# Optimization experiments

Measured on AMD Instinct MI355X. Metric: run time of the kernel, lower is better.

The kernel has to match this reference:

```python
import jax, jax.numpy as jnp
import numpy as np

B, N, D, DN, F, NUM_F, O, H = 8, 4096, 256, 128, 128, 1024, 8, 1024
EPS = 1e-5

def setup_inputs() -> dict:
    key = jax.random.key(0)
    ks = jax.random.split(key, 10)
    s = 0.02
    x = jax.random.normal(ks[0], (B, N, D), dtype=jnp.float32)
    ctx = jax.random.normal(ks[1], (B, DN), dtype=jnp.float32)
    idx = jax.random.randint(ks[2], (F,), 0, NUM_F, dtype=jnp.int64)
    cond_w = jax.random.normal(ks[3], (DN, 2 * D), dtype=jnp.float32) * s
    cond_b = jnp.zeros((2 * D,), dtype=jnp.float32)
    ffn_w_in = jax.random.normal(ks[4], (D, 2 * H), dtype=jnp.float32) * s
    ffn_b_in = jnp.zeros((2 * H,), dtype=jnp.float32)
    ffn_w_out = jax.random.normal(ks[5], (H, D), dtype=jnp.float32) * s
    ffn_b_out = jnp.zeros((D,), dtype=jnp.float32)
    emb = jax.random.normal(ks[6], (NUM_F, D * O), dtype=jnp.float32) * s
    return {"x": x, "ctx": ctx, "idx": idx, "cond_w": cond_w, "cond_b": cond_b,
            "ffn_w_in": ffn_w_in, "ffn_b_in": ffn_b_in,
            "ffn_w_out": ffn_w_out, "ffn_b_out": ffn_b_out, "emb": emb}

def reference(x, ctx, idx, cond_w, cond_b, ffn_w_in, ffn_b_in, ffn_w_out, ffn_b_out, emb):
    # Conditional LayerNorm: normalize over last dim, FiLM-style modulation from ctx
    mu = jnp.mean(x, axis=-1, keepdims=True)
    var = jnp.mean((x - mu) ** 2, axis=-1, keepdims=True)
    h = (x - mu) * jax.lax.rsqrt(var + EPS)                      # [B,N,D]
    ss = ctx @ cond_w + cond_b                                   # [B,2D]
    scale, shift = jnp.split(ss, 2, axis=-1)                     # [B,D] each
    h = h * (1.0 + scale[:, None, :]) + shift[:, None, :]
    # Gated FFN: in-proj -> (gelu(gate) * value) -> out-proj
    uv = h @ ffn_w_in + ffn_b_in                                 # [B,N,2H]
    u, v = jnp.split(uv, 2, axis=-1)
    y = (jax.nn.gelu(u) * v) @ ffn_w_out + ffn_b_out             # [B,N,D]
    # Embedding-generated per-feature output weights, then batched contraction
    w = emb[idx].reshape(F, D, O)                                # gather [F,D,O]
    out = jnp.einsum('bnd,fdo->bnfo', y, w)                      # [B,N,F,O]
    return out
```

## Files before the change

kernel.cpp:

```cpp
#include <hip/hip_runtime.h>
#include <cstdint>
#include <cstddef>

#define M_TOT 32768
#define D_    256
#define DN_   128
#define TWO_D 512
#define H_    1024
#define TWO_H 2048

typedef unsigned short ushort_t;
typedef __attribute__((ext_vector_type(8))) short bf16x8;
typedef __attribute__((ext_vector_type(4))) float f32x4;

__device__ __forceinline__ ushort_t f2bf(float f) {
  union { float f; uint32_t i; } v; v.f = f;
  uint32_t r = v.i + 0x7fffu + ((v.i >> 16) & 1u);
  return (ushort_t)(r >> 16);
}

__device__ __forceinline__ void async_ld16(const void* g, void* l) {
  __builtin_amdgcn_global_load_lds(
      (const __attribute__((address_space(1))) void*)g,
      (__attribute__((address_space(3))) void*)l, 16, 0, 0);
}

__global__ __launch_bounds__(256) void cond_ss_kernel(
    const float* __restrict__ ctx, const float* __restrict__ cond_w,
    const float* __restrict__ cond_b, float* __restrict__ ss) {
  int j = blockIdx.x * 256 + threadIdx.x;
  int b = j >> 9, col = j & 511;
  float acc = cond_b[col];
  for (int k = 0; k < DN_; ++k)
    acc += ctx[b * DN_ + k] * cond_w[k * TWO_D + col];
  ss[j] = acc;
}

__global__ __launch_bounds__(256) void transpose_f32_bf16_kernel(
    const float* __restrict__ in, ushort_t* __restrict__ out, int R, int C) {
  __shared__ float T[64 * 65];
  int ctiles = C >> 6;
  int bi = blockIdx.x / ctiles, bj = blockIdx.x % ctiles;
  int r0 = bi * 64, c0 = bj * 64;
  int tid = threadIdx.x;
#pragma unroll
  for (int it = 0; it < 16; ++it) {
    int idx = it * 256 + tid;
    int r = idx >> 6, c = idx & 63;
    T[r * 65 + c] = in[(size_t)(r0 + r) * C + c0 + c];
  }
  __syncthreads();
#pragma unroll
  for (int it = 0; it < 8; ++it) {
    int idx = it * 256 + tid;
    int a = idx >> 5;
    int b = (idx & 31) * 2;
    uint32_t pk = (uint32_t)f2bf(T[b * 65 + a]) |
                  ((uint32_t)f2bf(T[(b + 1) * 65 + a]) << 16);
    *(uint32_t*)&out[(size_t)(c0 + a) * R + r0 + b] = pk;
  }
}

__global__ __launch_bounds__(256) void gather_emb_kernel(
    const float* __restrict__ emb, const int* __restrict__ idx,
    ushort_t* __restrict__ W2T) {
  int f = blockIdx.x;
  bool looks64 = (idx[1] == 0) & (idx[3] == 0) & (idx[5] == 0) & (idx[7] == 0);
  int fi = looks64 ? idx[2 * f] : idx[f];
  const float* src = emb + (size_t)fi * 2048;
  int o = threadIdx.x >> 5, d0 = (threadIdx.x & 31) * 8;
  ushort_t buf[8];
#pragma unroll
  for (int k = 0; k < 8; ++k) buf[k] = f2bf(src[(d0 + k) * 8 + o]);
  *(bf16x8*)&W2T[(size_t)(f * 8 + o) * 256 + d0] = *(bf16x8*)buf;
}

__global__ __launch_bounds__(256) void ln_film_kernel(
    const float* __restrict__ x, const float* __restrict__ ss,
    ushort_t* __restrict__ h) {
  int row = blockIdx.x * 4 + (threadIdx.x >> 6);
  int lane = threadIdx.x & 63;
  int b = row >> 12;
  const float* xr = x + (size_t)row * D_;
  float4 pk = *(const float4*)(xr + lane * 4);
  float f0 = pk.x, f1 = pk.y, f2 = pk.z, f3 = pk.w;
  float s = f0 + f1 + f2 + f3;
  float q = f0 * f0 + f1 * f1 + f2 * f2 + f3 * f3;
#pragma unroll
  for (int off = 32; off > 0; off >>= 1) {
    s += __shfl_xor(s, off, 64);
    q += __shfl_xor(q, off, 64);
  }
  float mean = s * (1.0f / 256.0f);
  float var = q * (1.0f / 256.0f) - mean * mean;
  float rs = rsqrtf(var + 1e-5f);
  int d = lane * 4;
  const float* ssb = ss + b * TWO_D;
  float o0 = (f0 - mean) * rs * (1.0f + ssb[d + 0]) + ssb[256 + d + 0];
  float o1 = (f1 - mean) * rs * (1.0f + ssb[d + 1]) + ssb[256 + d + 1];
  float o2 = (f2 - mean) * rs * (1.0f + ssb[d + 2]) + ssb[256 + d + 2];
  float o3 = (f3 - mean) * rs * (1.0f + ssb[d + 3]) + ssb[256 + d + 3];
  uint2 st;
  st.x = (uint32_t)f2bf(o0) | ((uint32_t)f2bf(o1) << 16);
  st.y = (uint32_t)f2bf(o2) | ((uint32_t)f2bf(o3) << 16);
  *(uint2*)(h + (size_t)row * D_ + lane * 4) = st;
}

__global__ __launch_bounds__(256, 2) void ffn_fused_kernel(
    const ushort_t* __restrict__ h,
    const ushort_t* __restrict__ WinT,
    const float* __restrict__ bin,
    const ushort_t* __restrict__ WoutT,
    const float* __restrict__ bout,
    ushort_t* __restrict__ y) {
  __shared__ ushort_t Sh[2][16384];
  __shared__ ushort_t Gs[64 * 72];
  const int tid = threadIdx.x, lane = tid & 63, wave = tid >> 6;
  const int r = lane >> 2, q = lane & 3;
  const int l15 = lane & 15, l4 = lane >> 4;
  const int m0 = blockIdx.x * 64;
  const int fragoff = l15 * 32 + l4 * 8;

  const char* winp  = (const char*)WinT  + (wave * 16 + r) * 512 + q * 16;
  const char* woutp = (const char*)WoutT + (size_t)wave * 32768 + r * 2048 + q * 16;

  const ushort_t* hp = h + (size_t)(m0 + wave * 16 + l15) * 256 + l4 * 8;
  bf16x8 a_reg[8];
#pragma unroll
  for (int kc = 0; kc < 8; ++kc) a_reg[kc] = *(const bf16x8*)(hp + kc * 32);

#pragma unroll
  for (int i = 0; i < 4; ++i) {
    int t = i * 4 + wave;
    async_ld16(winp + i * 64,          &Sh[0][t * 512]);
    async_ld16(winp + i * 64 + 524288, &Sh[0][(16 + t) * 512]);
  }

  f32x4 yac[16] = {};
  int pb = 0;

  for (int j = 0; j < 16; ++j) {
    const int jb = j * 32768;
    f32x4 uac[4] = {}, vac[4] = {};

    asm volatile("s_waitcnt vmcnt(0)" ::: "memory");
    __builtin_amdgcn_s_barrier();
    asm volatile("" ::: "memory");
    {
      ushort_t* nxt = Sh[pb ^ 1];
#pragma unroll
      for (int i = 0; i < 4; ++i) {
        int t = i * 4 + wave;
        async_ld16(winp + jb + 256 + i * 64,          &nxt[t * 512]);
        async_ld16(winp + jb + 256 + i * 64 + 524288, &nxt[(16 + t) * 512]);
      }
      const ushort_t* cur = Sh[pb];
      __builtin_amdgcn_s_setprio(1);
#pragma unroll
      for (int ks = 0; ks < 4; ++ks) {
        bf16x8 af = a_reg[ks];
#pragma unroll
        for (int jt = 0; jt < 4; ++jt) {
          bf16x8 bu = *(const bf16x8*)&cur[(ks * 4 + jt) * 512 + fragoff];
          bf16x8 bv = *(const bf16x8*)&cur[(16 + ks * 4 + jt) * 512 + fragoff];
          uac[jt] = __builtin_amdgcn_mfma_f32_16x16x32_bf16(af, bu, uac[jt], 0, 0, 0);
          vac[jt] = __builtin_amdgcn_mfma_f32_16x16x32_bf16(af, bv, vac[jt], 0, 0, 0);
        }
      }
      __builtin_amdgcn_s_setprio(0);
    }
    pb ^= 1;

    asm volatile("s_waitcnt vmcnt(0)" ::: "memory");
    __builtin_amdgcn_s_barrier();
    asm volatile("" ::: "memory");
    {
      ushort_t* nxt = Sh[pb ^ 1];
#pragma unroll
      for (int i = 0; i < 4; ++i) {
        int t = i * 4 + wave;
        async_ld16(woutp + (size_t)i * 131072 + j * 128,      &nxt[t * 512]);
        async_ld16(woutp + (size_t)i * 131072 + j * 128 + 64, &nxt[(16 + t) * 512]);
      }
      const ushort_t* cur = Sh[pb];
      __builtin_amdgcn_s_setprio(1);
#pragma unroll
      for (int ks = 0; ks < 4; ++ks) {
        bf16x8 af = a_reg[4 + ks];
#pragma unroll
        for (int jt = 0; jt < 4; ++jt) {
          bf16x8 bu = *(const bf16x8*)&cur[(ks * 4 + jt) * 512 + fragoff];
          bf16x8 bv = *(const bf16x8*)&cur[(16 + ks * 4 + jt) * 512 + fragoff];
          uac[jt] = __builtin_amdgcn_mfma_f32_16x16x32_bf16(af, bu, uac[jt], 0, 0, 0);
          vac[jt] = __builtin_amdgcn_mfma_f32_16x16x32_bf16(af, bv, vac[jt], 0, 0, 0);
        }
      }
      __builtin_amdgcn_s_setprio(0);
    }
    pb ^= 1;

    asm volatile("s_waitcnt vmcnt(0)" ::: "memory");
    __builtin_amdgcn_s_barrier();
    asm volatile("" ::: "memory");
    if (j < 15) {
      ushort_t* nxt = Sh[pb ^ 1];
#pragma unroll
      for (int i = 0; i < 4; ++i) {
        int t = i * 4 + wave;
        async_ld16(winp + jb + 32768 + i * 64,          &nxt[t * 512]);
        async_ld16(winp + jb + 32768 + i * 64 + 524288, &nxt[(16 + t) * 512]);
      }
    }
#pragma unroll
    for (int jt = 0; jt < 4; ++jt) {
      int col = jt * 16 + l15;
      float bub = bin[j * 64 + col];
      float bvb = bin[1024 + j * 64 + col];
#pragma unroll
      for (int rr = 0; rr < 4; ++rr) {
        float u = uac[jt][rr] + bub;
        float v = vac[jt][rr] + bvb;
        float t = 0.7978845608028654f * (u + 0.044715f * u * u * u);
        float e = __expf(2.0f * t);
        float th = 1.0f - 2.0f / (e + 1.0f);
        float gl = 0.5f * u * (1.0f + th);
        Gs[(wave * 16 + l4 * 4 + rr) * 72 + col] = f2bf(gl * v);
      }
    }
    {
      const ushort_t* cur = Sh[pb];
#pragma unroll
      for (int s2 = 0; s2 < 2; ++s2) {
        bf16x8 gf = *(const bf16x8*)&Gs[(wave * 16 + l15) * 72 + s2 * 32 + l4 * 8];
        __builtin_amdgcn_s_setprio(1);
#pragma unroll
        for (int nt = 0; nt < 16; ++nt) {
          bf16x8 bw = *(const bf16x8*)&cur[(s2 * 16 + nt) * 512 + fragoff];
          yac[nt] = __builtin_amdgcn_mfma_f32_16x16x32_bf16(gf, bw, yac[nt], 0, 0, 0);
        }
        __builtin_amdgcn_s_setprio(0);
      }
    }
    pb ^= 1;
  }

  asm volatile("s_waitcnt vmcnt(0)" ::: "memory");
  __builtin_amdgcn_s_barrier();
  asm volatile("" ::: "memory");
  ushort_t* E = &Sh[0][0];
#pragma unroll
  for (int nt = 0; nt < 16; ++nt) {
    int col = nt * 16 + l15;
    float bb = bout[col];
#pragma unroll
    for (int rr = 0; rr < 4; ++rr)
      E[(wave * 16 + l4 * 4 + rr) * 264 + col] = f2bf(yac[nt][rr] + bb);
  }
  asm volatile("s_waitcnt lgkmcnt(0)" ::: "memory");
  __builtin_amdgcn_s_barrier();
  asm volatile("" ::: "memory");
#pragma unroll
  for (int it = 0; it < 8; ++it) {
    int id = it * 256 + tid;
    int rr = id >> 5, cc = id & 31;
    bf16x8 vv = *(const bf16x8*)&E[rr * 264 + cc * 8];
    *(bf16x8*)&y[(size_t)(m0 + rr) * 256 + cc * 8] = vv;
  }
}

__global__ __launch_bounds__(256, 2) void gemm_out_kernel(
    const ushort_t* __restrict__ A, const ushort_t* __restrict__ BT,
    float* __restrict__ C) {
  __shared__ ushort_t As[128 * 64];
  __shared__ ushort_t Bs[128 * 64];
  __shared__ float Cs[64 * 132];
  const int tid = threadIdx.x, lane = tid & 63, wave = tid >> 6;
  const int wm = wave >> 1, wn = wave & 1;
  const int m0 = blockIdx.x * 128, n0 = blockIdx.y * 128;
  const int r = lane >> 2, q = lane & 3;
  const int l15 = lane & 15, l4 = lane >> 4;
  const int fragoff = l15 * 32 + l4 * 8;
  const int N = 1024, K = 256;
  f32x4 acc[4][4] = {};
  for (int k0 = 0; k0 < K; k0 += 64) {
    for (int t = wave; t < 16; t += 4) {
      int rt = t >> 1, ks = t & 1;
      async_ld16(A + (size_t)(m0 + rt * 16 + r) * K + k0 + ks * 32 + q * 8, &As[t * 512]);
      async_ld16(BT + (size_t)(n0 + rt * 16 + r) * K + k0 + ks * 32 + q * 8, &Bs[t * 512]);
    }
    __syncthreads();
#pragma unroll
    for (int ks = 0; ks < 2; ++ks) {
      bf16x8 a[4], b[4];
#pragma unroll
      for (int i = 0; i < 4; ++i)
        a[i] = *(const bf16x8*)&As[((wm * 4 + i) * 2 + ks) * 512 + fragoff];
#pragma unroll
      for (int jt = 0; jt < 4; ++jt)
        b[jt] = *(const bf16x8*)&Bs[((wn * 4 + jt) * 2 + ks) * 512 + fragoff];
#pragma unroll
      for (int i = 0; i < 4; ++i)
#pragma unroll
        for (int jt = 0; jt < 4; ++jt)
          acc[i][jt] = __builtin_amdgcn_mfma_f32_16x16x32_bf16(a[i], b[jt], acc[i][jt], 0, 0, 0);
    }
    __syncthreads();
  }
#pragma unroll
  for (int p = 0; p < 2; ++p) {
    __syncthreads();
    if (wm == p) {
#pragma unroll
      for (int jt = 0; jt < 4; ++jt) {
        int col = wn * 64 + jt * 16 + l15;
#pragma unroll
        for (int i = 0; i < 4; ++i) {
          int rl = i * 16 + (l4 << 2);
#pragma unroll
          for (int rr = 0; rr < 4; ++rr)
            Cs[(rl + rr) * 132 + col] = acc[i][jt][rr];
        }
      }
    }
    __syncthreads();
#pragma unroll
    for (int it = 0; it < 8; ++it) {
      int t = it * 256 + tid;
      int rr = t >> 5, c = (t & 31) * 4;
      float4 v = *(const float4*)&Cs[rr * 132 + c];
      *(float4*)&C[(size_t)(m0 + p * 64 + rr) * N + n0 + c] = v;
    }
  }
}

extern "C" void kernel_launch(void* const* d_in, const int* in_sizes, int n_in,
                              void* d_out, int out_size, void* d_ws, size_t ws_size,
                              hipStream_t stream) {
  const float* x      = (const float*)d_in[0];
  const float* ctx    = (const float*)d_in[1];
  const int*   idx    = (const int*)d_in[2];
  const float* cond_w = (const float*)d_in[3];
  const float* cond_b = (const float*)d_in[4];
  const float* w_in   = (const float*)d_in[5];
  const float* b_in   = (const float*)d_in[6];
  const float* w_out  = (const float*)d_in[7];
  const float* b_out  = (const float*)d_in[8];
  const float* emb    = (const float*)d_in[9];

  char* w = (char*)d_ws;
  float* ss = (float*)w;           w += (size_t)8 * TWO_D * 4;
  ushort_t* h = (ushort_t*)w;      w += (size_t)M_TOT * D_ * 2;
  ushort_t* y = (ushort_t*)w;      w += (size_t)M_TOT * D_ * 2;
  ushort_t* WinT = (ushort_t*)w;   w += (size_t)TWO_H * D_ * 2;
  ushort_t* WoutT = (ushort_t*)w;  w += (size_t)D_ * H_ * 2;
  ushort_t* W2T = (ushort_t*)w;    w += (size_t)H_ * D_ * 2;

  cond_ss_kernel<<<16, 256, 0, stream>>>(ctx, cond_w, cond_b, ss);
  transpose_f32_bf16_kernel<<<(D_ / 64) * (TWO_H / 64), 256, 0, stream>>>(w_in, WinT, D_, TWO_H);
  transpose_f32_bf16_kernel<<<(H_ / 64) * (D_ / 64), 256, 0, stream>>>(w_out, WoutT, H_, D_);
  gather_emb_kernel<<<128, 256, 0, stream>>>(emb, idx, W2T);
  ln_film_kernel<<<M_TOT / 4, 256, 0, stream>>>(x, ss, h);
  ffn_fused_kernel<<<M_TOT / 64, 256, 0, stream>>>(h, WinT, b_in, WoutT, b_out, y);
  gemm_out_kernel<<<dim3(M_TOT / 128, H_ / 128), 256, 0, stream>>>(y, W2T, (float*)d_out);
}
```

Measured before the change: 299.1 us.

## Retile fused FFN waves as 2x2 and XOR-swizzle LDS fragment layout

The fused FFN kernel now assigns each wave a 32-row by half-width tile in a 2x2 wave grid instead of 16 rows by full width. Each B fragment read from LDS then feeds two MFMAs, which halves the LDS reads per MFMA. Both the FFN and output GEMM kernels apply an XOR swizzle to the 16-byte chunk position on async load and fragment read, to reduce LDS bank conflicts. In exchange, register pressure rises from doubled A fragments, and an extra barrier is needed because waves now read gated-activation rows written by other waves.

```diff
diff --git a/kernel.cpp b/kernel.cpp
--- a/kernel.cpp
+++ b/kernel.cpp
@@ -116,18 +116,23 @@
   __shared__ ushort_t Sh[2][16384];
   __shared__ ushort_t Gs[64 * 72];
   const int tid = threadIdx.x, lane = tid & 63, wave = tid >> 6;
+  const int wm = wave >> 1, wn = wave & 1;
   const int r = lane >> 2, q = lane & 3;
+  const int qs = q ^ ((r >> 1) & 3);
   const int l15 = lane & 15, l4 = lane >> 4;
   const int m0 = blockIdx.x * 64;
-  const int fragoff = l15 * 32 + l4 * 8;
-
-  const char* winp  = (const char*)WinT  + (wave * 16 + r) * 512 + q * 16;
-  const char* woutp = (const char*)WoutT + (size_t)wave * 32768 + r * 2048 + q * 16;
-
-  const ushort_t* hp = h + (size_t)(m0 + wave * 16 + l15) * 256 + l4 * 8;
-  bf16x8 a_reg[8];
-#pragma unroll
-  for (int kc = 0; kc < 8; ++kc) a_reg[kc] = *(const bf16x8*)(hp + kc * 32);
+  const int fragoff = l15 * 32 + (l4 ^ ((l15 >> 1) & 3)) * 8;
+
+  const char* winp  = (const char*)WinT  + (wave * 16 + r) * 512 + qs * 16;
+  const char* woutp = (const char*)WoutT + (size_t)wave * 32768 + r * 2048 + qs * 16;
+
+  const ushort_t* hp = h + (size_t)(m0 + wm * 32 + l15) * 256 + l4 * 8;
+  bf16x8 a_reg[2][8];
+#pragma unroll
+  for (int rt = 0; rt < 2; ++rt)
+#pragma unroll
+    for (int kc = 0; kc < 8; ++kc)
+      a_reg[rt][kc] = *(const bf16x8*)(hp + rt * 4096 + kc * 32);
 
 #pragma unroll
   for (int i = 0; i < 4; ++i) {
@@ -136,12 +141,12 @@
     async_ld16(winp + i * 64 + 524288, &Sh[0][(16 + t) * 512]);
   }
 
-  f32x4 yac[16] = {};
+  f32x4 yac[2][8] = {};
   int pb = 0;
 
   for (int j = 0; j < 16; ++j) {
     const int jb = j * 32768;
-    f32x4 uac[4] = {}, vac[4] = {};
+    f32x4 uac[2][2] = {}, vac[2][2] = {};
 
     asm volatile("s_waitcnt vmcnt(0)" ::: "memory");
     __builtin_amdgcn_s_barrier();
@@ -158,13 +163,15 @@
       __builtin_amdgcn_s_setprio(1);
 #pragma unroll
       for (int ks = 0; ks < 4; ++ks) {
-        bf16x8 af = a_reg[ks];
-#pragma unroll
-        for (int jt = 0; jt < 4; ++jt) {
-          bf16x8 bu = *(const bf16x8*)&cur[(ks * 4 + jt) * 512 + fragoff];
-          bf16x8 bv = *(const bf16x8*)&cur[(16 + ks * 4 + jt) * 512 + fragoff];
-          uac[jt] = __builtin_amdgcn_mfma_f32_16x16x32_bf16(af, bu, uac[jt], 0, 0, 0);
-          vac[jt] = __builtin_amdgcn_mfma_f32_16x16x32_bf16(af, bv, vac[jt], 0, 0, 0);
+#pragma unroll
+        for (int jj = 0; jj < 2; ++jj) {
+          int t = ks * 4 + wn * 2 + jj;
+          bf16x8 bu = *(const bf16x8*)&cur[t * 512 + fragoff];
+          bf16x8 bv = *(const bf16x8*)&cur[(16 + t) * 512 + fragoff];
+          uac[0][jj] = __builtin_amdgcn_mfma_f32_16x16x32_bf16(a_reg[0][ks], bu, uac[0][jj], 0, 0, 0);
+          uac[1][jj] = __builtin_amdgcn_mfma_f32_16x16x32_bf16(a_reg[1][ks], bu, uac[1][jj], 0, 0, 0);
+          vac[0][jj] = __builtin_amdgcn_mfma_f32_16x16x32_bf16(a_reg[0][ks], bv, vac[0][jj], 0, 0, 0);
+          vac[1][jj] = __builtin_amdgcn_mfma_f32_16x16x32_bf16(a_reg[1][ks], bv, vac[1][jj], 0, 0, 0);
         }
       }
       __builtin_amdgcn_s_setprio(0);
@@ -186,13 +193,15 @@
       __builtin_amdgcn_s_setprio(1);
 #pragma unroll
       for (int ks = 0; ks < 4; ++ks) {
-        bf16x8 af = a_reg[4 + ks];
-#pragma unroll
-        for (int jt = 0; jt < 4; ++jt) {
-          bf16x8 bu = *(const bf16x8*)&cur[(ks * 4 + jt) * 512 + fragoff];
-          bf16x8 bv = *(const bf16x8*)&cur[(16 + ks * 4 + jt) * 512 + fragoff];
-          uac[jt] = __builtin_amdgcn_mfma_f32_16x16x32_bf16(af, bu, uac[jt], 0, 0, 0);
-          vac[jt] = __builtin_amdgcn_mfma_f32_16x16x32_bf16(af, bv, vac[jt], 0, 0, 0);
+#pragma unroll
+        for (int jj = 0; jj < 2; ++jj) {
+          int t = ks * 4 + wn * 2 + jj;
+          bf16x8 bu = *(const bf16x8*)&cur[t * 512 + fragoff];
+          bf16x8 bv = *(const bf16x8*)&cur[(16 + t) * 512 + fragoff];
+          uac[0][jj] = __builtin_amdgcn_mfma_f32_16x16x32_bf16(a_reg[0][4 + ks], bu, uac[0][jj], 0, 0, 0);
+          uac[1][jj] = __builtin_amdgcn_mfma_f32_16x16x32_bf16(a_reg[1][4 + ks], bu, uac[1][jj], 0, 0, 0);
+          vac[0][jj] = __builtin_amdgcn_mfma_f32_16x16x32_bf16(a_reg[0][4 + ks], bv, vac[0][jj], 0, 0, 0);
+          vac[1][jj] = __builtin_amdgcn_mfma_f32_16x16x32_bf16(a_reg[1][4 + ks], bv, vac[1][jj], 0, 0, 0);
         }
       }
       __builtin_amdgcn_s_setprio(0);
@@ -212,31 +221,40 @@
       }
     }
 #pragma unroll
-    for (int jt = 0; jt < 4; ++jt) {
-      int col = jt * 16 + l15;
-      float bub = bin[j * 64 + col];
-      float bvb = bin[1024 + j * 64 + col];
-#pragma unroll
-      for (int rr = 0; rr < 4; ++rr) {
-        float u = uac[jt][rr] + bub;
-        float v = vac[jt][rr] + bvb;
-        float t = 0.7978845608028654f * (u + 0.044715f * u * u * u);
-        float e = __expf(2.0f * t);
-        float th = 1.0f - 2.0f / (e + 1.0f);
-        float gl = 0.5f * u * (1.0f + th);
-        Gs[(wave * 16 + l4 * 4 + rr) * 72 + col] = f2bf(gl * v);
-      }
-    }
+    for (int jj = 0; jj < 2; ++jj) {
+      int gcol = wn * 32 + jj * 16 + l15;
+      float bub = bin[j * 64 + gcol];
+      float bvb = bin[1024 + j * 64 + gcol];
+#pragma unroll
+      for (int rt = 0; rt < 2; ++rt) {
+#pragma unroll
+        for (int rr = 0; rr < 4; ++rr) {
+          float u = uac[rt][jj][rr] + bub;
+          float v = vac[rt][jj][rr] + bvb;
+          float t = 0.7978845608028654f * (u + 0.044715f * u * u * u);
+          float e = __expf(2.0f * t);
+          float th = 1.0f - 2.0f / (e + 1.0f);
+          float gl = 0.5f * u * (1.0f + th);
+          Gs[(wm * 32 + rt * 16 + l4 * 4 + rr) * 72 + gcol] = f2bf(gl * v);
+        }
+      }
+    }
+    asm volatile("s_waitcnt lgkmcnt(0)" ::: "memory");
+    __builtin_amdgcn_s_barrier();
+    asm volatile("" ::: "memory");
     {
       const ushort_t* cur = Sh[pb];
 #pragma unroll
       for (int s2 = 0; s2 < 2; ++s2) {
-        bf16x8 gf = *(const bf16x8*)&Gs[(wave * 16 + l15) * 72 + s2 * 32 + l4 * 8];
+        bf16x8 gf0 = *(const bf16x8*)&Gs[(wm * 32 + l15) * 72 + s2 * 32 + l4 * 8];
+        bf16x8 gf1 = *(const bf16x8*)&Gs[(wm * 32 + 16 + l15) * 72 + s2 * 32 + l4 * 8];
         __builtin_amdgcn_s_setprio(1);
 #pragma unroll
-        for (int nt = 0; nt < 16; ++nt) {
-          bf16x8 bw = *(const bf16x8*)&cur[(s2 * 16 + nt) * 512 + fragoff];
-          yac[nt] = __builtin_amdgcn_mfma_f32_16x16x32_bf16(gf, bw, yac[nt], 0, 0, 0);
+        for (int nt8 = 0; nt8 < 8; ++nt8) {
+          int t = s2 * 16 + wn * 8 + nt8;
+          bf16x8 bw = *(const bf16x8*)&cur[t * 512 + fragoff];
+          yac[0][nt8] = __builtin_amdgcn_mfma_f32_16x16x32_bf16(gf0, bw, yac[0][nt8], 0, 0, 0);
+          yac[1][nt8] = __builtin_amdgcn_mfma_f32_16x16x32_bf16(gf1, bw, yac[1][nt8], 0, 0, 0);
         }
         __builtin_amdgcn_s_setprio(0);
       }
@@ -249,12 +267,15 @@
   asm volatile("" ::: "memory");
   ushort_t* E = &Sh[0][0];
 #pragma unroll
-  for (int nt = 0; nt < 16; ++nt) {
-    int col = nt * 16 + l15;
+  for (int nt8 = 0; nt8 < 8; ++nt8) {
+    int col = wn * 128 + nt8 * 16 + l15;
     float bb = bout[col];
 #pragma unroll
-    for (int rr = 0; rr < 4; ++rr)
-      E[(wave * 16 + l4 * 4 + rr) * 264 + col] = f2bf(yac[nt][rr] + bb);
+    for (int rt = 0; rt < 2; ++rt) {
+#pragma unroll
+      for (int rr = 0; rr < 4; ++rr)
+        E[(wm * 32 + rt * 16 + l4 * 4 + rr) * 264 + col] = f2bf(yac[rt][nt8][rr] + bb);
+    }
   }
   asm volatile("s_waitcnt lgkmcnt(0)" ::: "memory");
   __builtin_amdgcn_s_barrier();
@@ -278,15 +299,16 @@
   const int wm = wave >> 1, wn = wave & 1;
   const int m0 = blockIdx.x * 128, n0 = blockIdx.y * 128;
   const int r = lane >> 2, q = lane & 3;
+  const int qs = q ^ ((r >> 1) & 3);
   const int l15 = lane & 15, l4 = lane >> 4;
-  const int fragoff = l15 * 32 + l4 * 8;
+  const int fragoff = l15 * 32 + (l4 ^ ((l15 >> 1) & 3)) * 8;
   const int N = 1024, K = 256;
   f32x4 acc[4][4] = {};
   for (int k0 = 0; k0 < K; k0 += 64) {
     for (int t = wave; t < 16; t += 4) {
       int rt = t >> 1, ks = t & 1;
-      async_ld16(A + (size_t)(m0 + rt * 16 + r) * K + k0 + ks * 32 + q * 8, &As[t * 512]);
-      async_ld16(BT + (size_t)(n0 + rt * 16 + r) * K + k0 + ks * 32 + q * 8, &Bs[t * 512]);
+      async_ld16(A + (size_t)(m0 + rt * 16 + r) * K + k0 + ks * 32 + qs * 8, &As[t * 512]);
+      async_ld16(BT + (size_t)(n0 + rt * 16 + r) * K + k0 + ks * 32 + qs * 8, &Bs[t * 512]);
     }
     __syncthreads();
 #pragma unroll
```

Measured after the change: 288.7 us. 3.4% less time.
